# Performance work log

Hardware: AMD Instinct MI355X
Metric: run time of the kernel (lower is better)

## Reference

```python
import jax, jax.numpy as jnp
import numpy as np

EPS = 1e-5


def _conv_w(x, k):
    # cross-correlation along width, kernel size 2, padding 1 -> width W+1
    xp = jnp.pad(x, ((0, 0), (0, 0), (0, 0), (1, 1)))
    return k[0] * xp[..., :-1] + k[1] * xp[..., 1:]


def _conv_h(x, k):
    # cross-correlation along height, kernel size 2, padding 1 -> height H+1
    xp = jnp.pad(x, ((0, 0), (0, 0), (1, 1), (0, 0)))
    return k[0] * xp[..., :-1, :] + k[1] * xp[..., 1:, :]


def _dwt(x, lp, hp):
    L = _conv_h(_conv_w(x, lp), lp)
    Hc = _conv_h(_conv_w(x, hp), hp)
    return L[:, :, ::2, ::2], Hc[:, :, ::2, ::2]


def _bn(y, g, b, m, v):
    # eval-mode batchnorm over channel axis 1
    scale = (g / jnp.sqrt(v + EPS))[None, :, None, None]
    shift = (b - m * g / jnp.sqrt(v + EPS))[None, :, None, None]
    return y * scale + shift


def setup_inputs() -> dict:
    key = jax.random.key(0)
    ks = jax.random.split(key, 8)
    S, B, H, W, C = 5, 8, 512, 512, 64
    x = jax.random.normal(ks[0], (B, 1, H, W), dtype=jnp.float32)
    lp = jnp.tile(jnp.array([0.7071, 0.7071], dtype=jnp.float32), (S, 1))
    hp = jnp.tile(jnp.array([0.7071, -0.7071], dtype=jnp.float32), (S, 1))
    w1 = jax.random.normal(ks[1], (S, C, 1), dtype=jnp.float32) * 0.5
    w2 = jax.random.normal(ks[2], (S, C, C), dtype=jnp.float32) * (1.0 / np.sqrt(C))
    g1 = jnp.ones((S, C), jnp.float32)
    b1 = jnp.zeros((S, C), jnp.float32)
    m1 = jax.random.normal(ks[3], (S, C), dtype=jnp.float32) * 0.1
    v1 = jax.random.uniform(ks[4], (S, C), dtype=jnp.float32) + 0.5
    g2 = jnp.ones((S, C), jnp.float32)
    b2 = jnp.zeros((S, C), jnp.float32)
    m2 = jax.random.normal(ks[5], (S, C), dtype=jnp.float32) * 0.1
    v2 = jax.random.uniform(ks[6], (S, C), dtype=jnp.float32) + 0.5
    return dict(x=x, lp=lp, hp=hp, w1=w1, w2=w2, g1=g1, b1=b1, m1=m1, v1=v1,
                g2=g2, b2=b2, m2=m2, v2=v2)


def reference(x, lp, hp, w1, w2, g1, b1, m1, v1, g2, b2, m2, v2):
    # Returns stacked-over-scale (L, H_coeff, processed_L):
    #   L, Hc: [S, B, 1, H', W'];  P: [S, B, 64, H', W']
    def per_scale(lp_s, hp_s, w1_s, g1_s, b1_s, m1_s, v1_s,
                  w2_s, g2_s, b2_s, m2_s, v2_s):
        L, Hc = _dwt(x, lp_s, hp_s)
        y = jnp.einsum('oc,bchw->bohw', w1_s, L)
        y = jax.nn.relu(_bn(y, g1_s, b1_s, m1_s, v1_s))
        y = jnp.einsum('oc,bchw->bohw', w2_s, y)
        y = jax.nn.relu(_bn(y, g2_s, b2_s, m2_s, v2_s))
        return L, Hc, y

    return jax.vmap(per_scale)(lp, hp, w1, g1, b1, m1, v1, w2, g2, b2, m2, v2)
```

## Files before the change

kernel.cpp:

```cpp
#include <hip/hip_runtime.h>
#include <math.h>

#define EPSF 1e-5f

constexpr int Sn = 5, Bn = 8, Hin = 512, Win = 512, Cn = 64;
constexpr int HO = 257, WO = 257;
constexpr int HW = HO * WO;
constexpr int NPIX = Bn * HW;
constexpr int TOTPIX = Sn * NPIX;
constexpr int NSB = Sn * Bn;
constexpr int HWP = (HW + 3) & ~3;

constexpr int    WSF    = 64 + Cn * 66 * 2;
constexpr size_t LR_OFF = (size_t)Sn * WSF;
constexpr unsigned PTOTu = (unsigned)((long)NSB * Cn * HW);
constexpr size_t WS_NEED = (LR_OFF + (size_t)NSB * HWP * 2) * 4;

typedef float f32x4 __attribute__((ext_vector_type(4)));
typedef f32x4 f32x4u __attribute__((aligned(8)));

__global__ __launch_bounds__(64) void precompute_kernel(
    const float* __restrict__ w1, const float* __restrict__ w2,
    const float* __restrict__ g1, const float* __restrict__ b1,
    const float* __restrict__ m1, const float* __restrict__ v1,
    const float* __restrict__ g2, const float* __restrict__ b2,
    const float* __restrict__ m2, const float* __restrict__ v2,
    float* __restrict__ ws) {
    int s = blockIdx.x;
    int c = threadIdx.x;
    __shared__ float sa1[Cn], st1[Cn], stc[Cn], stS[Cn];
    __shared__ int   scS[Cn];

    int idx = s * Cn + c;
    float sc1 = g1[idx] / sqrtf(v1[idx] + EPSF);
    float a1  = sc1 * w1[idx];
    float t1  = b1[idx] - m1[idx] * sc1;
    sa1[c] = a1;
    st1[c] = t1;
    float tc = (a1 != 0.f) ? (-t1 / a1) : INFINITY;
    stc[c] = tc;
    __syncthreads();

    int rk = 0;
    for (int c2 = 0; c2 < Cn; c2++) {
        float t = stc[c2];
        rk += (t < tc) || (t == tc && c2 < c);
    }
    stS[rk] = tc;
    scS[rk] = c;
    __syncthreads();

    float* wss = ws + (size_t)s * WSF;
    wss[c] = stS[c];

    int o = c;
    float sc2 = g2[idx] / sqrtf(v2[idx] + EPSF);
    float t2o = b2[idx] - m2[idx] * sc2;
    const float* w2row = w2 + ((size_t)s * Cn + o) * Cn;

    float alpha = 0.f, beta = t2o;
    for (int cc = 0; cc < Cn; cc++) {
        float a = sa1[cc];
        bool act = (a < 0.f) || (a == 0.f && st1[cc] > 0.f);
        if (act) {
            float wf = sc2 * w2row[cc];
            alpha = fmaf(wf, a, alpha);
            beta  = fmaf(wf, st1[cc], beta);
        }
    }
    float2* abrow = (float2*)(wss + Cn);
    abrow[o * 66 + 0] = make_float2(alpha, beta);

    for (int r = 1; r <= Cn; r++) {
        int cc = scS[r - 1];
        float a = sa1[cc];
        if (a != 0.f) {
            float wf = sc2 * w2row[cc];
            float sgn = (a > 0.f) ? 1.f : -1.f;
            alpha = fmaf(sgn * wf, a, alpha);
            beta  = fmaf(sgn * wf, st1[cc], beta);
        }
        abrow[o * 66 + r] = make_float2(alpha, beta);
    }
}

constexpr int GPT = 4;
constexpr int TPB = 256;
constexpr int PIXPB = TPB * GPT;
constexpr int NCHUNK = (HW + PIXPB - 1) / PIXPB;

__device__ __forceinline__ float pwl(const float2 ab, float v) {
    return fmaxf(fmaf(ab.x, v, ab.y), 0.f);
}

__device__ __forceinline__ void dwt_lh(
    const float* __restrict__ xb, int i, int j,
    float l0, float l1, float h0, float h1,
    float& Lq, float& Hq) {
    const int r0 = 2 * i - 1, r1 = 2 * i;
    const int c0 = 2 * j - 1, c1 = 2 * j;
    const float x00 = (r0 >= 0 && r0 < Hin && c0 >= 0 ) ? xb[r0 * Win + c0] : 0.f;
    const float x01 = (r0 >= 0 && r0 < Hin && c1 < Win) ? xb[r0 * Win + c1] : 0.f;
    const float x10 = (r1 < Hin && c0 >= 0 )            ? xb[r1 * Win + c0] : 0.f;
    const float x11 = (r1 < Hin && c1 < Win)            ? xb[r1 * Win + c1] : 0.f;
    Lq = l0 * (l0 * x00 + l1 * x01) + l1 * (l0 * x10 + l1 * x11);
    Hq = h0 * (h0 * x00 + h1 * x01) + h1 * (h0 * x10 + h1 * x11);
}

template <bool WITH_LR>
__global__ __launch_bounds__(TPB) void dwt_kernel(
    const float* __restrict__ x,
    const float* __restrict__ lp, const float* __restrict__ hp,
    const float* __restrict__ ws_tab,
    float* __restrict__ Lout, float* __restrict__ Hout,
    float* __restrict__ lrws) {
    __shared__ float stS[Cn];
    const int tid = threadIdx.x;
    const int b = blockIdx.y, s = blockIdx.z;
    if (WITH_LR) {
        if (tid < Cn) stS[tid] = ws_tab[(size_t)s * WSF + tid];
        __syncthreads();
    }

    const float l0 = lp[2 * s], l1 = lp[2 * s + 1];
    const float h0 = hp[2 * s], h1 = hp[2 * s + 1];
    const float* xb = x + (size_t)b * (Hin * Win);

    const int pbase = (blockIdx.x * TPB + tid) * GPT;

    float Lv[GPT + 3];
    float Hv[GPT + 3];
    int   rr[GPT];

    int i = pbase / WO;
    int j = pbase - i * WO;
    #pragma unroll
    for (int q = 0; q < GPT; ++q) {
        dwt_lh(xb, i, j, l0, l1, h0, h1, Lv[q], Hv[q]);
        if (WITH_LR) {
            int lo = 0, hi = Cn;
            while (lo < hi) {
                const int mid = (lo + hi) >> 1;
                if (stS[mid] < Lv[q]) lo = mid + 1; else hi = mid;
            }
            rr[q] = lo;
        }
        if (++j == WO) { j = 0; ++i; }
    }
    Lv[4] = __shfl_down(Lv[0], 1, 64);  Hv[4] = __shfl_down(Hv[0], 1, 64);
    Lv[5] = __shfl_down(Lv[1], 1, 64);  Hv[5] = __shfl_down(Hv[1], 1, 64);
    Lv[6] = __shfl_down(Lv[2], 1, 64);  Hv[6] = __shfl_down(Hv[2], 1, 64);
    if ((tid & 63) == 63) {
        #pragma unroll
        for (int q = GPT; q < GPT + 3; ++q) {
            dwt_lh(xb, i, j, l0, l1, h0, h1, Lv[q], Hv[q]);
            if (++j == WO) { j = 0; ++i; }
        }
    }

    const int sb = s * Bn + b;
    const size_t lb = (size_t)sb * HW + pbase;
    const int dlt = (4 - (sb & 3)) & 3;
    const bool fast = (pbase + GPT + 3 <= HW);

    if (fast) {
        f32x4 l4, h4;
        switch (dlt) {
            case 0:  l4 = f32x4{Lv[0], Lv[1], Lv[2], Lv[3]};
                     h4 = f32x4{Hv[0], Hv[1], Hv[2], Hv[3]}; break;
            case 1:  l4 = f32x4{Lv[1], Lv[2], Lv[3], Lv[4]};
                     h4 = f32x4{Hv[1], Hv[2], Hv[3], Hv[4]}; break;
            case 2:  l4 = f32x4{Lv[2], Lv[3], Lv[4], Lv[5]};
                     h4 = f32x4{Hv[2], Hv[3], Hv[4], Hv[5]}; break;
            default: l4 = f32x4{Lv[3], Lv[4], Lv[5], Lv[6]};
                     h4 = f32x4{Hv[3], Hv[4], Hv[5], Hv[6]}; break;
        }
        *(f32x4*)(Lout + lb + dlt) = l4;
        __builtin_nontemporal_store(h4, (f32x4*)(Hout + lb + dlt));
        if (pbase == 0) {
            if (dlt > 0) { Lout[lb + 0] = Lv[0]; Hout[lb + 0] = Hv[0]; }
            if (dlt > 1) { Lout[lb + 1] = Lv[1]; Hout[lb + 1] = Hv[1]; }
            if (dlt > 2) { Lout[lb + 2] = Lv[2]; Hout[lb + 2] = Hv[2]; }
        }
    } else {
        #pragma unroll
        for (int q = 0; q < GPT; ++q) {
            if (pbase + q < HW) {
                Lout[lb + q] = Lv[q];
                Hout[lb + q] = Hv[q];
            }
        }
    }

    if (WITH_LR) {
        float2* lr = (float2*)lrws + (size_t)sb * HWP + pbase;
        if (fast) {
            f32x4 p01 = f32x4{Lv[0], (float)rr[0], Lv[1], (float)rr[1]};
            f32x4 p23 = f32x4{Lv[2], (float)rr[2], Lv[3], (float)rr[3]};
            *(f32x4*)(lr)     = p01;
            *(f32x4*)(lr + 2) = p23;
        } else {
            #pragma unroll
            for (int q = 0; q < GPT; ++q) {
                if (pbase + q < HW) lr[q] = make_float2(Lv[q], (float)rr[q]);
            }
        }
    }
}

constexpr int EPB = TPB * 16;
constexpr unsigned NBLK2 = (PTOTu + EPB - 1) / EPB;

__global__ __launch_bounds__(TPB) void pstore_flat(
    const float* __restrict__ ws_tab,
    const float* __restrict__ lrws,
    float* __restrict__ Pout) {
    __shared__ float2 tabs[2][66];

    const int tid = threadIdx.x;
    const unsigned base = (unsigned)blockIdx.x * (unsigned)EPB;
    const unsigned plane_first = base / (unsigned)HW;
    unsigned lastf = base + (unsigned)(EPB - 1);
    if (lastf >= PTOTu) lastf = PTOTu - 1u;
    const unsigned plane_last = lastf / (unsigned)HW;

    if (tid < 132) {
        const int slot = (tid >= 66);
        const int idx  = slot ? tid - 66 : tid;
        const unsigned pl = slot ? plane_last : plane_first;
        const int s = pl >> 9;
        const int o = pl & 63;
        const float2* row =
            (const float2*)(ws_tab + (size_t)s * WSF + Cn) + (size_t)o * 66;
        tabs[slot][idx] = row[idx];
    }
    __syncthreads();

    const float2* LR = (const float2*)lrws;

    #pragma unroll
    for (int k = 0; k < 4; ++k) {
        const unsigned flat = base + (unsigned)k * (TPB * 4u) + (unsigned)tid * 4u;
        if (flat >= PTOTu) break;
        const unsigned plane = flat / (unsigned)HW;
        const unsigned px0   = flat - plane * (unsigned)HW;
        const int row = (plane != plane_first);

        if (px0 <= (unsigned)(HW - 4) && flat + 3u < PTOTu) {
            const float2* lr = LR + (size_t)(plane >> 6) * HWP + px0;
            const f32x4u v01 = *(const f32x4u*)(lr);
            const f32x4u v23 = *(const f32x4u*)(lr + 2);
            const float2 ab0 = tabs[row][(int)v01.y];
            const float2 ab1 = tabs[row][(int)v01.w];
            const float2 ab2 = tabs[row][(int)v23.y];
            const float2 ab3 = tabs[row][(int)v23.w];
            f32x4 outv;
            outv.x = pwl(ab0, v01.x);
            outv.y = pwl(ab1, v01.z);
            outv.z = pwl(ab2, v23.x);
            outv.w = pwl(ab3, v23.z);
            __builtin_nontemporal_store(outv, (f32x4*)(Pout + flat));
        } else {
            #pragma unroll
            for (int e = 0; e < 4; ++e) {
                const unsigned fe = flat + (unsigned)e;
                if (fe >= PTOTu) break;
                const unsigned pl = fe / (unsigned)HW;
                const unsigned px = fe - pl * (unsigned)HW;
                const int rw = (pl != plane_first);
                const float2 lrv = LR[(size_t)(pl >> 6) * HWP + px];
                const float2 ab  = tabs[rw][(int)lrv.y];
                Pout[fe] = pwl(ab, lrv.x);
            }
        }
    }
}

__global__ __launch_bounds__(TPB) void pstore_v5(
    const float* __restrict__ Lin,
    const float* __restrict__ ws,
    float* __restrict__ Pout) {
    __shared__ float  stS[Cn];
    __shared__ float2 sab[4 * 66];

    const int tid = threadIdx.x;
    const int og  = blockIdx.y;
    const int sb  = blockIdx.z;
    const int s   = sb >> 3;

    const float* wss = ws + (size_t)s * WSF;
    if (tid < Cn) stS[tid] = wss[tid];
    const float2* abg = (const float2*)(wss + Cn) + (size_t)og * 4 * 66;
    for (int t = tid; t < 4 * 66; t += TPB) sab[t] = abg[t];
    __syncthreads();

    const int p4 = (blockIdx.x * TPB + tid) * GPT;
    const float* Lp = Lin + (size_t)sb * HW;

    float Lv[GPT + 3];
    int   lo7[GPT + 3];

    #pragma unroll
    for (int q = 0; q < GPT; ++q) {
        const int px = p4 + q;
        const float Lq = (px < HW) ? Lp[px] : 0.f;
        Lv[q] = Lq;
        int lo = 0, hi = Cn;
        while (lo < hi) {
            const int mid = (lo + hi) >> 1;
            if (stS[mid] < Lq) lo = mid + 1; else hi = mid;
        }
        lo7[q] = lo;
    }
    Lv[4] = __shfl_down(Lv[0], 1, 64);  lo7[4] = __shfl_down(lo7[0], 1, 64);
    Lv[5] = __shfl_down(Lv[1], 1, 64);  lo7[5] = __shfl_down(lo7[1], 1, 64);
    Lv[6] = __shfl_down(Lv[2], 1, 64);  lo7[6] = __shfl_down(lo7[2], 1, 64);
    if ((tid & 63) == 63) {
        #pragma unroll
        for (int q = GPT; q < GPT + 3; ++q) {
            const int px = p4 + q;
            const float Lq = (px < HW) ? Lp[px] : 0.f;
            Lv[q] = Lq;
            int lo = 0, hi = Cn;
            while (lo < hi) {
                const int mid = (lo + hi) >> 1;
                if (stS[mid] < Lq) lo = mid + 1; else hi = mid;
            }
            lo7[q] = lo;
        }
    }

    float* const Pb = Pout + ((size_t)sb * Cn + (size_t)og * 4) * HW;

    if (p4 + GPT + 3 <= HW) {
        {   f32x4 v = f32x4{pwl(sab[0 * 66 + lo7[0]], Lv[0]),
                            pwl(sab[0 * 66 + lo7[1]], Lv[1]),
                            pwl(sab[0 * 66 + lo7[2]], Lv[2]),
                            pwl(sab[0 * 66 + lo7[3]], Lv[3])};
            *(f32x4*)(Pb + p4) = v; }
        {   f32x4 v = f32x4{pwl(sab[1 * 66 + lo7[3]], Lv[3]),
                            pwl(sab[1 * 66 + lo7[4]], Lv[4]),
                            pwl(sab[1 * 66 + lo7[5]], Lv[5]),
                            pwl(sab[1 * 66 + lo7[6]], Lv[6])};
            *(f32x4*)(Pb + (size_t)HW + p4 + 3) = v; }
        {   f32x4 v = f32x4{pwl(sab[2 * 66 + lo7[2]], Lv[2]),
                            pwl(sab[2 * 66 + lo7[3]], Lv[3]),
                            pwl(sab[2 * 66 + lo7[4]], Lv[4]),
                            pwl(sab[2 * 66 + lo7[5]], Lv[5])};
            *(f32x4*)(Pb + 2 * (size_t)HW + p4 + 2) = v; }
        {   f32x4 v = f32x4{pwl(sab[3 * 66 + lo7[1]], Lv[1]),
                            pwl(sab[3 * 66 + lo7[2]], Lv[2]),
                            pwl(sab[3 * 66 + lo7[3]], Lv[3]),
                            pwl(sab[3 * 66 + lo7[4]], Lv[4])};
            *(f32x4*)(Pb + 3 * (size_t)HW + p4 + 1) = v; }
        if (p4 == 0) {
            Pb[1 * (size_t)HW + 0] = pwl(sab[1 * 66 + lo7[0]], Lv[0]);
            Pb[1 * (size_t)HW + 1] = pwl(sab[1 * 66 + lo7[1]], Lv[1]);
            Pb[1 * (size_t)HW + 2] = pwl(sab[1 * 66 + lo7[2]], Lv[2]);
            Pb[2 * (size_t)HW + 0] = pwl(sab[2 * 66 + lo7[0]], Lv[0]);
            Pb[2 * (size_t)HW + 1] = pwl(sab[2 * 66 + lo7[1]], Lv[1]);
            Pb[3 * (size_t)HW + 0] = pwl(sab[3 * 66 + lo7[0]], Lv[0]);
        }
    } else {
        #pragma unroll
        for (int q = 0; q < GPT; ++q) {
            const int px = p4 + q;
            if (px >= HW) break;
            const float Lq = Lv[q];
            const int   r  = lo7[q];
            Pb[0 * (size_t)HW + px] = pwl(sab[0 * 66 + r], Lq);
            Pb[1 * (size_t)HW + px] = pwl(sab[1 * 66 + r], Lq);
            Pb[2 * (size_t)HW + px] = pwl(sab[2 * 66 + r], Lq);
            Pb[3 * (size_t)HW + px] = pwl(sab[3 * 66 + r], Lq);
        }
    }
}

extern "C" void kernel_launch(void* const* d_in, const int* in_sizes, int n_in,
                              void* d_out, int out_size, void* d_ws, size_t ws_size,
                              hipStream_t stream) {
    const float* x  = (const float*)d_in[0];
    const float* lp = (const float*)d_in[1];
    const float* hp = (const float*)d_in[2];
    const float* w1 = (const float*)d_in[3];
    const float* w2 = (const float*)d_in[4];
    const float* g1 = (const float*)d_in[5];
    const float* b1 = (const float*)d_in[6];
    const float* m1 = (const float*)d_in[7];
    const float* v1 = (const float*)d_in[8];
    const float* g2 = (const float*)d_in[9];
    const float* b2 = (const float*)d_in[10];
    const float* m2 = (const float*)d_in[11];
    const float* v2 = (const float*)d_in[12];

    float* out  = (float*)d_out;
    float* Lout = out;
    float* Hout = out + TOTPIX;
    float* Pout = out + 2 * TOTPIX;
    float* ws   = (float*)d_ws;

    precompute_kernel<<<Sn, Cn, 0, stream>>>(w1, w2, g1, b1, m1, v1,
                                             g2, b2, m2, v2, ws);

    dim3 grid1(NCHUNK, Bn, Sn);

    if (ws_size >= WS_NEED) {
        float* lrws = ws + LR_OFF;
        dwt_kernel<true><<<grid1, TPB, 0, stream>>>(x, lp, hp, ws,
                                                    Lout, Hout, lrws);
        pstore_flat<<<dim3(NBLK2), TPB, 0, stream>>>(ws, lrws, Pout);
    } else {
        dwt_kernel<false><<<grid1, TPB, 0, stream>>>(x, lp, hp, ws,
                                                     Lout, Hout, nullptr);
        dim3 grid2(NCHUNK, Cn / 4, Sn * Bn);
        pstore_v5<<<grid2, TPB, 0, stream>>>(Lout, ws, Pout);
    }
}
```

Before: 736.4 us.

## Route L and H outputs through workspace and write all outputs in one flat pass

The DWT kernel now writes only packed (L, bin index) pairs and H values to padded workspace buffers, dropping the misaligned halo/shuffle stores into the final output. A single flat store kernel then writes L, H and P into the contiguous output with aligned 16-byte nontemporal stores. This aims to make every output write aligned and coalesced, at the cost of an extra workspace write and read for H and L.

```diff
diff --git a/kernel.cpp b/kernel.cpp
--- a/kernel.cpp
+++ b/kernel.cpp
@@ -11,10 +11,15 @@
 constexpr int NSB = Sn * Bn;
 constexpr int HWP = (HW + 3) & ~3;
 
+constexpr unsigned U_TOTPIX = (unsigned)TOTPIX;
+constexpr unsigned U_TWOT   = 2u * U_TOTPIX;
+constexpr unsigned PTOTu    = (unsigned)((long)NSB * Cn * HW);
+constexpr unsigned U_TOT    = U_TWOT + PTOTu;
+
 constexpr int    WSF    = 64 + Cn * 66 * 2;
 constexpr size_t LR_OFF = (size_t)Sn * WSF;
-constexpr unsigned PTOTu = (unsigned)((long)NSB * Cn * HW);
-constexpr size_t WS_NEED = (LR_OFF + (size_t)NSB * HWP * 2) * 4;
+constexpr size_t H_OFF  = LR_OFF + (size_t)NSB * HWP * 2;
+constexpr size_t WS_NEED = (H_OFF + (size_t)NSB * HWP) * 4;
 
 typedef float f32x4 __attribute__((ext_vector_type(4)));
 typedef f32x4 f32x4u __attribute__((aligned(8)));
@@ -107,44 +112,222 @@
     Hq = h0 * (h0 * x00 + h1 * x01) + h1 * (h0 * x10 + h1 * x11);
 }
 
-template <bool WITH_LR>
-__global__ __launch_bounds__(TPB) void dwt_kernel(
+__global__ __launch_bounds__(TPB) void dwt_pack(
     const float* __restrict__ x,
     const float* __restrict__ lp, const float* __restrict__ hp,
     const float* __restrict__ ws_tab,
-    float* __restrict__ Lout, float* __restrict__ Hout,
-    float* __restrict__ lrws) {
+    float* __restrict__ lrws, float* __restrict__ hws) {
     __shared__ float stS[Cn];
     const int tid = threadIdx.x;
     const int b = blockIdx.y, s = blockIdx.z;
-    if (WITH_LR) {
-        if (tid < Cn) stS[tid] = ws_tab[(size_t)s * WSF + tid];
-        __syncthreads();
-    }
+    if (tid < Cn) stS[tid] = ws_tab[(size_t)s * WSF + tid];
+    __syncthreads();
+
+    const int pbase = (blockIdx.x * TPB + tid) * GPT;
+    if (pbase >= HW) return;
 
     const float l0 = lp[2 * s], l1 = lp[2 * s + 1];
     const float h0 = hp[2 * s], h1 = hp[2 * s + 1];
     const float* xb = x + (size_t)b * (Hin * Win);
 
+    float Lv[GPT], Hv[GPT];
+    int   rr[GPT];
+
+    int i = pbase / WO;
+    int j = pbase - i * WO;
+    #pragma unroll
+    for (int q = 0; q < GPT; ++q) {
+        if (pbase + q < HW) {
+            dwt_lh(xb, i, j, l0, l1, h0, h1, Lv[q], Hv[q]);
+            int lo = 0, hi = Cn;
+            while (lo < hi) {
+                const int mid = (lo + hi) >> 1;
+                if (stS[mid] < Lv[q]) lo = mid + 1; else hi = mid;
+            }
+            rr[q] = lo;
+        } else { Lv[q] = 0.f; Hv[q] = 0.f; rr[q] = 0; }
+        if (++j == WO) { j = 0; ++i; }
+    }
+
+    const int sb = s * Bn + b;
+    float2* lr = (float2*)lrws + (size_t)sb * HWP + pbase;
+    float*  hp_ = hws + (size_t)sb * HWP + pbase;
+
+    if (pbase + GPT <= HW) {
+        f32x4 p01 = f32x4{Lv[0], (float)rr[0], Lv[1], (float)rr[1]};
+        f32x4 p23 = f32x4{Lv[2], (float)rr[2], Lv[3], (float)rr[3]};
+        *(f32x4*)(lr)     = p01;
+        *(f32x4*)(lr + 2) = p23;
+        *(f32x4*)(hp_)    = f32x4{Hv[0], Hv[1], Hv[2], Hv[3]};
+    } else {
+        #pragma unroll
+        for (int q = 0; q < GPT; ++q) {
+            if (pbase + q < HW) {
+                lr[q]  = make_float2(Lv[q], (float)rr[q]);
+                hp_[q] = Hv[q];
+            }
+        }
+    }
+}
+
+constexpr int EPB = TPB * 16;
+constexpr unsigned NBLK2 = (U_TOT + EPB - 1) / EPB;
+
+__global__ __launch_bounds__(TPB) void store_flat(
+    const float* __restrict__ ws_tab,
+    const float* __restrict__ lrws,
+    const float* __restrict__ hws,
+    float* __restrict__ out) {
+    __shared__ float2 tabs[2][66];
+
+    const int tid = threadIdx.x;
+    const unsigned base = (unsigned)blockIdx.x * (unsigned)EPB;
+    const float2* LR = (const float2*)lrws;
+
+    if (base + EPB <= U_TOTPIX) {
+        #pragma unroll
+        for (int k = 0; k < 4; ++k) {
+            const unsigned f = base + (unsigned)k * (TPB * 4u) + (unsigned)tid * 4u;
+            const unsigned sb  = f / (unsigned)HW;
+            const unsigned px0 = f - sb * (unsigned)HW;
+            if (px0 <= (unsigned)(HW - 4)) {
+                const float2* lr = LR + (size_t)sb * HWP + px0;
+                const f32x4u v01 = *(const f32x4u*)(lr);
+                const f32x4u v23 = *(const f32x4u*)(lr + 2);
+                f32x4 v; v.x = v01.x; v.y = v01.z; v.z = v23.x; v.w = v23.z;
+                __builtin_nontemporal_store(v, (f32x4*)(out + f));
+            } else {
+                #pragma unroll
+                for (int e = 0; e < 4; ++e) {
+                    const unsigned fe = f + (unsigned)e;
+                    const unsigned s2 = fe / (unsigned)HW;
+                    const unsigned px = fe - s2 * (unsigned)HW;
+                    out[fe] = LR[(size_t)s2 * HWP + px].x;
+                }
+            }
+        }
+        return;
+    }
+    if (base >= U_TOTPIX && base + EPB <= U_TWOT) {
+        #pragma unroll
+        for (int k = 0; k < 4; ++k) {
+            const unsigned f = base + (unsigned)k * (TPB * 4u) + (unsigned)tid * 4u;
+            const unsigned g = f - U_TOTPIX;
+            const unsigned sb  = g / (unsigned)HW;
+            const unsigned px0 = g - sb * (unsigned)HW;
+            if (px0 <= (unsigned)(HW - 4)) {
+                const float* hp_ = hws + (size_t)sb * HWP + px0;
+                f32x4 v; v.x = hp_[0]; v.y = hp_[1]; v.z = hp_[2]; v.w = hp_[3];
+                __builtin_nontemporal_store(v, (f32x4*)(out + f));
+            } else {
+                #pragma unroll
+                for (int e = 0; e < 4; ++e) {
+                    const unsigned ge = g + (unsigned)e;
+                    const unsigned s2 = ge / (unsigned)HW;
+                    const unsigned px = ge - s2 * (unsigned)HW;
+                    out[U_TOTPIX + ge] = hws[(size_t)s2 * HWP + px];
+                }
+            }
+        }
+        return;
+    }
+    if (base >= U_TWOT && base + EPB <= U_TOT) {
+        const unsigned qbase = base - U_TWOT;
+        const unsigned plane_first = qbase / (unsigned)HW;
+        const unsigned plane_last  = (qbase + (unsigned)(EPB - 1)) / (unsigned)HW;
+        if (tid < 132) {
+            const int slot = (tid >= 66);
+            const int idx  = slot ? tid - 66 : tid;
+            const unsigned pl = slot ? plane_last : plane_first;
+            const int s = (int)(pl >> 9);
+            const int o = (int)(pl & 63u);
+            const float2* row =
+                (const float2*)(ws_tab + (size_t)s * WSF + Cn) + (size_t)o * 66;
+            tabs[slot][idx] = row[idx];
+        }
+        __syncthreads();
+
+        #pragma unroll
+        for (int k = 0; k < 4; ++k) {
+            const unsigned q = qbase + (unsigned)k * (TPB * 4u) + (unsigned)tid * 4u;
+            const unsigned plane = q / (unsigned)HW;
+            const unsigned px0   = q - plane * (unsigned)HW;
+            const int row = (plane != plane_first);
+            if (px0 <= (unsigned)(HW - 4)) {
+                const float2* lr = LR + (size_t)(plane >> 6) * HWP + px0;
+                const f32x4u v01 = *(const f32x4u*)(lr);
+                const f32x4u v23 = *(const f32x4u*)(lr + 2);
+                const float2 ab0 = tabs[row][(int)v01.y];
+                const float2 ab1 = tabs[row][(int)v01.w];
+                const float2 ab2 = tabs[row][(int)v23.y];
+                const float2 ab3 = tabs[row][(int)v23.w];
+                f32x4 v;
+                v.x = pwl(ab0, v01.x);
+                v.y = pwl(ab1, v01.z);
+                v.z = pwl(ab2, v23.x);
+                v.w = pwl(ab3, v23.z);
+                __builtin_nontemporal_store(v, (f32x4*)(out + U_TWOT + q));
+            } else {
+                #pragma unroll
+                for (int e = 0; e < 4; ++e) {
+                    const unsigned qe = q + (unsigned)e;
+                    const unsigned pl = qe / (unsigned)HW;
+                    const unsigned px = qe - pl * (unsigned)HW;
+                    const int rw = (pl != plane_first);
+                    const float2 lrv = LR[(size_t)(pl >> 6) * HWP + px];
+                    const float2 ab  = tabs[rw][(int)lrv.y];
+                    out[U_TWOT + qe] = pwl(ab, lrv.x);
+                }
+            }
+        }
+        return;
+    }
+    for (int k = 0; k < 16; ++k) {
+        const unsigned f = base + (unsigned)k * (unsigned)TPB + (unsigned)tid;
+        if (f >= U_TOT) return;
+        if (f < U_TOTPIX) {
+            const unsigned sb = f / (unsigned)HW;
+            const unsigned px = f - sb * (unsigned)HW;
+            out[f] = LR[(size_t)sb * HWP + px].x;
+        } else if (f < U_TWOT) {
+            const unsigned g  = f - U_TOTPIX;
+            const unsigned sb = g / (unsigned)HW;
+            const unsigned px = g - sb * (unsigned)HW;
+            out[f] = hws[(size_t)sb * HWP + px];
+        } else {
+            const unsigned q  = f - U_TWOT;
+            const unsigned pl = q / (unsigned)HW;
+            const unsigned px = q - pl * (unsigned)HW;
+            const int s = (int)(pl >> 9);
+            const int o = (int)(pl & 63u);
+            const float2 lrv = LR[(size_t)(pl >> 6) * HWP + px];
+            const float2 ab  = ((const float2*)(ws_tab + (size_t)s * WSF + Cn))
+                                   [(size_t)o * 66 + (int)lrv.y];
+            out[f] = pwl(ab, lrv.x);
+        }
+    }
+}
+
+__global__ __launch_bounds__(TPB) void dwt_halo(
+    const float* __restrict__ x,
+    const float* __restrict__ lp, const float* __restrict__ hp,
+    float* __restrict__ Lout, float* __restrict__ Hout) {
+    const int tid = threadIdx.x;
+    const int b = blockIdx.y, s = blockIdx.z;
+
+    const float l0 = lp[2 * s], l1 = lp[2 * s + 1];
+    const float h0 = hp[2 * s], h1 = hp[2 * s + 1];
+    const float* xb = x + (size_t)b * (Hin * Win);
+
     const int pbase = (blockIdx.x * TPB + tid) * GPT;
-
-    float Lv[GPT + 3];
-    float Hv[GPT + 3];
-    int   rr[GPT];
-
+    if (pbase >= HW) return;
+
+    float Lv[GPT + 3], Hv[GPT + 3];
     int i = pbase / WO;
     int j = pbase - i * WO;
     #pragma unroll
     for (int q = 0; q < GPT; ++q) {
         dwt_lh(xb, i, j, l0, l1, h0, h1, Lv[q], Hv[q]);
-        if (WITH_LR) {
-            int lo = 0, hi = Cn;
-            while (lo < hi) {
-                const int mid = (lo + hi) >> 1;
-                if (stS[mid] < Lv[q]) lo = mid + 1; else hi = mid;
-            }
-            rr[q] = lo;
-        }
         if (++j == WO) { j = 0; ++i; }
     }
     Lv[4] = __shfl_down(Lv[0], 1, 64);  Hv[4] = __shfl_down(Hv[0], 1, 64);
@@ -188,89 +371,6 @@
             if (pbase + q < HW) {
                 Lout[lb + q] = Lv[q];
                 Hout[lb + q] = Hv[q];
-            }
-        }
-    }
-
-    if (WITH_LR) {
-        float2* lr = (float2*)lrws + (size_t)sb * HWP + pbase;
-        if (fast) {
-            f32x4 p01 = f32x4{Lv[0], (float)rr[0], Lv[1], (float)rr[1]};
-            f32x4 p23 = f32x4{Lv[2], (float)rr[2], Lv[3], (float)rr[3]};
-            *(f32x4*)(lr)     = p01;
-            *(f32x4*)(lr + 2) = p23;
-        } else {
-            #pragma unroll
-            for (int q = 0; q < GPT; ++q) {
-                if (pbase + q < HW) lr[q] = make_float2(Lv[q], (float)rr[q]);
-            }
-        }
-    }
-}
-
-constexpr int EPB = TPB * 16;
-constexpr unsigned NBLK2 = (PTOTu + EPB - 1) / EPB;
-
-__global__ __launch_bounds__(TPB) void pstore_flat(
-    const float* __restrict__ ws_tab,
-    const float* __restrict__ lrws,
-    float* __restrict__ Pout) {
-    __shared__ float2 tabs[2][66];
-
-    const int tid = threadIdx.x;
-    const unsigned base = (unsigned)blockIdx.x * (unsigned)EPB;
-    const unsigned plane_first = base / (unsigned)HW;
-    unsigned lastf = base + (unsigned)(EPB - 1);
-    if (lastf >= PTOTu) lastf = PTOTu - 1u;
-    const unsigned plane_last = lastf / (unsigned)HW;
-
-    if (tid < 132) {
-        const int slot = (tid >= 66);
-        const int idx  = slot ? tid - 66 : tid;
-        const unsigned pl = slot ? plane_last : plane_first;
-        const int s = pl >> 9;
-        const int o = pl & 63;
-        const float2* row =
-            (const float2*)(ws_tab + (size_t)s * WSF + Cn) + (size_t)o * 66;
-        tabs[slot][idx] = row[idx];
-    }
-    __syncthreads();
-
-    const float2* LR = (const float2*)lrws;
-
-    #pragma unroll
-    for (int k = 0; k < 4; ++k) {
-        const unsigned flat = base + (unsigned)k * (TPB * 4u) + (unsigned)tid * 4u;
-        if (flat >= PTOTu) break;
-        const unsigned plane = flat / (unsigned)HW;
-        const unsigned px0   = flat - plane * (unsigned)HW;
-        const int row = (plane != plane_first);
-
-        if (px0 <= (unsigned)(HW - 4) && flat + 3u < PTOTu) {
-            const float2* lr = LR + (size_t)(plane >> 6) * HWP + px0;
-            const f32x4u v01 = *(const f32x4u*)(lr);
-            const f32x4u v23 = *(const f32x4u*)(lr + 2);
-            const float2 ab0 = tabs[row][(int)v01.y];
-            const float2 ab1 = tabs[row][(int)v01.w];
-            const float2 ab2 = tabs[row][(int)v23.y];
-            const float2 ab3 = tabs[row][(int)v23.w];
-            f32x4 outv;
-            outv.x = pwl(ab0, v01.x);
-            outv.y = pwl(ab1, v01.z);
-            outv.z = pwl(ab2, v23.x);
-            outv.w = pwl(ab3, v23.z);
-            __builtin_nontemporal_store(outv, (f32x4*)(Pout + flat));
-        } else {
-            #pragma unroll
-            for (int e = 0; e < 4; ++e) {
-                const unsigned fe = flat + (unsigned)e;
-                if (fe >= PTOTu) break;
-                const unsigned pl = fe / (unsigned)HW;
-                const unsigned px = fe - pl * (unsigned)HW;
-                const int rw = (pl != plane_first);
-                const float2 lrv = LR[(size_t)(pl >> 6) * HWP + px];
-                const float2 ab  = tabs[rw][(int)lrv.y];
-                Pout[fe] = pwl(ab, lrv.x);
             }
         }
     }
@@ -406,12 +506,11 @@
 
     if (ws_size >= WS_NEED) {
         float* lrws = ws + LR_OFF;
-        dwt_kernel<true><<<grid1, TPB, 0, stream>>>(x, lp, hp, ws,
-                                                    Lout, Hout, lrws);
-        pstore_flat<<<dim3(NBLK2), TPB, 0, stream>>>(ws, lrws, Pout);
+        float* hws  = ws + H_OFF;
+        dwt_pack<<<grid1, TPB, 0, stream>>>(x, lp, hp, ws, lrws, hws);
+        store_flat<<<dim3(NBLK2), TPB, 0, stream>>>(ws, lrws, hws, out);
     } else {
-        dwt_kernel<false><<<grid1, TPB, 0, stream>>>(x, lp, hp, ws,
-                                                     Lout, Hout, nullptr);
+        dwt_halo<<<grid1, TPB, 0, stream>>>(x, lp, hp, Lout, Hout);
         dim3 grid2(NCHUNK, Cn / 4, Sn * Bn);
         pstore_v5<<<grid2, TPB, 0, stream>>>(Lout, ws, Pout);
     }
```

Result: no change. 733.1 us (-0.4%).
